# Performance work log

Hardware: AMD Instinct MI355X
Metric: run time of the kernel (lower is better)

## Reference

```python
import jax, jax.numpy as jnp
import numpy as np

B = 128          # batch of proteins
MAX_ATOMS = 16384  # padded max atoms per protein


def setup_inputs() -> dict:
    key = jax.random.key(0)
    k1, k2, k3 = jax.random.split(key, 3)
    # Coordinates are stored flat as [B, 3*MAX_ATOMS] like the torch module.
    inp = jax.random.normal(k1, (B, 3 * MAX_ATOMS), dtype=jnp.float32) * 10.0
    tgt = jax.random.normal(k2, (B, 3 * MAX_ATOMS), dtype=jnp.float32) * 10.0
    num_atoms = jax.random.randint(k3, (B,), MAX_ATOMS // 2, MAX_ATOMS + 1, dtype=jnp.int32)
    return {"input": inp, "target": tgt, "num_atoms": num_atoms}


def _kabsch_rmsd(x_flat, y_flat, num_atoms):
    """Per-batch optimal-superposition RMSD (Kabsch) with ragged atom counts.

    x_flat, y_flat: [B, 3*N] flat coords; num_atoms: [B] valid atoms per row.
    Uses the closed form rmsd^2 = (E0 - 2*(s0 + s1 + d*s2)) / n, where s are
    singular values of the 3x3 cross-covariance and d fixes reflections.
    """
    Bsz, N3 = x_flat.shape
    N = N3 // 3
    x = x_flat.reshape(Bsz, N, 3)
    y = y_flat.reshape(Bsz, N, 3)

    mask = (jnp.arange(N)[None, :] < num_atoms[:, None]).astype(x.dtype)[..., None]  # [B,N,1]
    cnt = num_atoms.astype(x.dtype)[:, None]  # [B,1]

    # Masked centroids and centered (masked) coords.
    xm = jnp.sum(x * mask, axis=1) / cnt  # [B,3]
    ym = jnp.sum(y * mask, axis=1) / cnt
    xc = (x - xm[:, None, :]) * mask      # [B,N,3], zero on padding
    yc = (y - ym[:, None, :]) * mask

    # 3x3 cross-covariance per protein.
    C = jnp.einsum('bni,bnj->bij', xc, yc)  # [B,3,3]

    U, S, Vt = jnp.linalg.svd(C)
    d = jnp.sign(jnp.linalg.det(U) * jnp.linalg.det(Vt))  # reflection correction
    sum_s = S[:, 0] + S[:, 1] + d * S[:, 2]

    E0 = jnp.sum(xc * xc, axis=(1, 2)) + jnp.sum(yc * yc, axis=(1, 2))
    msd = jnp.maximum(E0 - 2.0 * sum_s, 0.0) / cnt[:, 0]
    return jnp.sqrt(msd + 1e-8)  # tiny eps for gradient stability at msd==0


def reference(input, target, num_atoms):
    return _kabsch_rmsd(input, target, num_atoms)
```

## Files before the change

### kernel.cpp

```cpp
#include <hip/hip_runtime.h>

#define NPROT 128
#define NATOMS 16384
#define BLK_PER_PROT 4
#define THREADS 256
#define GROUPS_PER_BLOCK (NATOMS / BLK_PER_PROT / 4)
#define GROUPS_PER_THREAD (GROUPS_PER_BLOCK / THREADS)

__global__ __launch_bounds__(THREADS) void kabsch_reduce_kernel(
    const float* __restrict__ x, const float* __restrict__ y,
    const int* __restrict__ num_atoms, float* __restrict__ ws)
{
    const int b = blockIdx.x / BLK_PER_PROT;
    const int chunk = blockIdx.x % BLK_PER_PROT;
    const int na = num_atoms[b];
    const float4* px = (const float4*)(x + (size_t)b * 3 * NATOMS);
    const float4* py = (const float4*)(y + (size_t)b * 3 * NATOMS);

    float acc[17];
    #pragma unroll
    for (int i = 0; i < 17; ++i) acc[i] = 0.f;

    const int t = threadIdx.x;
    #pragma unroll
    for (int it = 0; it < GROUPS_PER_THREAD; ++it) {
        const int g = chunk * GROUPS_PER_BLOCK + it * THREADS + t;
        const float4 fx0 = px[3 * g + 0];
        const float4 fx1 = px[3 * g + 1];
        const float4 fx2 = px[3 * g + 2];
        const float4 fy0 = py[3 * g + 0];
        const float4 fy1 = py[3 * g + 1];
        const float4 fy2 = py[3 * g + 2];
        const int a0 = g * 4;
        const float xs[4][3] = {{fx0.x, fx0.y, fx0.z}, {fx0.w, fx1.x, fx1.y},
                                {fx1.z, fx1.w, fx2.x}, {fx2.y, fx2.z, fx2.w}};
        const float ys[4][3] = {{fy0.x, fy0.y, fy0.z}, {fy0.w, fy1.x, fy1.y},
                                {fy1.z, fy1.w, fy2.x}, {fy2.y, fy2.z, fy2.w}};
        #pragma unroll
        for (int k = 0; k < 4; ++k) {
            const float m = (a0 + k < na) ? 1.f : 0.f;
            const float X0 = xs[k][0] * m, X1 = xs[k][1] * m, X2 = xs[k][2] * m;
            const float Y0 = ys[k][0] * m, Y1 = ys[k][1] * m, Y2 = ys[k][2] * m;
            acc[0] += X0;  acc[1] += X1;  acc[2] += X2;
            acc[3] += Y0;  acc[4] += Y1;  acc[5] += Y2;
            acc[6]  += X0 * Y0;  acc[7]  += X0 * Y1;  acc[8]  += X0 * Y2;
            acc[9]  += X1 * Y0;  acc[10] += X1 * Y1;  acc[11] += X1 * Y2;
            acc[12] += X2 * Y0;  acc[13] += X2 * Y1;  acc[14] += X2 * Y2;
            acc[15] += X0 * X0 + X1 * X1 + X2 * X2;
            acc[16] += Y0 * Y0 + Y1 * Y1 + Y2 * Y2;
        }
    }

    #pragma unroll
    for (int i = 0; i < 17; ++i) {
        float v = acc[i];
        #pragma unroll
        for (int off = 32; off; off >>= 1) v += __shfl_down(v, off);
        acc[i] = v;
    }
    __shared__ float red[THREADS / 64][17];
    const int wave = t >> 6, lane = t & 63;
    if (lane == 0) {
        #pragma unroll
        for (int i = 0; i < 17; ++i) red[wave][i] = acc[i];
    }
    __syncthreads();
    if (t == 0) {
        float* dst = ws + ((size_t)b * BLK_PER_PROT + chunk) * 17;
        #pragma unroll
        for (int i = 0; i < 17; ++i)
            dst[i] = red[0][i] + red[1][i] + red[2][i] + red[3][i];
    }
}

__global__ __launch_bounds__(NPROT) void kabsch_finalize_kernel(
    const float* __restrict__ ws, const int* __restrict__ num_atoms,
    float* __restrict__ out)
{
    const int b = threadIdx.x;
    if (b >= NPROT) return;

    double s[17];
    #pragma unroll
    for (int i = 0; i < 17; ++i) s[i] = 0.0;
    for (int c = 0; c < BLK_PER_PROT; ++c) {
        const float* p = ws + ((size_t)b * BLK_PER_PROT + c) * 17;
        #pragma unroll
        for (int i = 0; i < 17; ++i) s[i] += (double)p[i];
    }

    const double n = (double)num_atoms[b];
    const double mx0 = s[0] / n, mx1 = s[1] / n, mx2 = s[2] / n;
    const double my0 = s[3] / n, my1 = s[4] / n, my2 = s[5] / n;

    double C00 = s[6]  - n * mx0 * my0, C01 = s[7]  - n * mx0 * my1, C02 = s[8]  - n * mx0 * my2;
    double C10 = s[9]  - n * mx1 * my0, C11 = s[10] - n * mx1 * my1, C12 = s[11] - n * mx1 * my2;
    double C20 = s[12] - n * mx2 * my0, C21 = s[13] - n * mx2 * my1, C22 = s[14] - n * mx2 * my2;

    const double E0 = (s[15] - n * (mx0 * mx0 + mx1 * mx1 + mx2 * mx2))
                    + (s[16] - n * (my0 * my0 + my1 * my1 + my2 * my2));

    const double a00 = C00 * C00 + C10 * C10 + C20 * C20;
    const double a01 = C00 * C01 + C10 * C11 + C20 * C21;
    const double a02 = C00 * C02 + C10 * C12 + C20 * C22;
    const double a11 = C01 * C01 + C11 * C11 + C21 * C21;
    const double a12 = C01 * C02 + C11 * C12 + C21 * C22;
    const double a22 = C02 * C02 + C12 * C12 + C22 * C22;

    const double p1 = a01 * a01 + a02 * a02 + a12 * a12;
    const double q = (a00 + a11 + a22) / 3.0;
    const double b00 = a00 - q, b11 = a11 - q, b22 = a22 - q;
    const double p2 = b00 * b00 + b11 * b11 + b22 * b22 + 2.0 * p1;
    double e0, e1, e2;
    if (p2 <= 0.0) {
        e0 = e1 = e2 = q;
    } else {
        const double p = sqrt(p2 / 6.0);
        const double inv = 1.0 / p;
        const double c00 = b00 * inv, c01 = a01 * inv, c02 = a02 * inv;
        const double c11 = b11 * inv, c12 = a12 * inv, c22 = b22 * inv;
        double r = 0.5 * (c00 * (c11 * c22 - c12 * c12)
                        - c01 * (c01 * c22 - c12 * c02)
                        + c02 * (c01 * c12 - c11 * c02));
        r = fmin(1.0, fmax(-1.0, r));
        const double phi = acos(r) / 3.0;
        e0 = q + 2.0 * p * cos(phi);
        e2 = q + 2.0 * p * cos(phi + 2.0943951023931953);
        e1 = 3.0 * q - e0 - e2;
    }
    const double s0 = sqrt(fmax(e0, 0.0));
    const double s1 = sqrt(fmax(e1, 0.0));
    const double s2 = sqrt(fmax(e2, 0.0));

    const double detC = C00 * (C11 * C22 - C12 * C21)
                      - C01 * (C10 * C22 - C12 * C20)
                      + C02 * (C10 * C21 - C11 * C20);
    const double sum_s = s0 + s1 + (detC < 0.0 ? -s2 : s2);

    const double msd = fmax(E0 - 2.0 * sum_s, 0.0) / n;
    out[b] = (float)sqrt(msd + 1e-8);
}

extern "C" void kernel_launch(void* const* d_in, const int* in_sizes, int n_in,
                              void* d_out, int out_size, void* d_ws, size_t ws_size,
                              hipStream_t stream) {
    const float* x = (const float*)d_in[0];
    const float* y = (const float*)d_in[1];
    const int* num_atoms = (const int*)d_in[2];
    float* out = (float*)d_out;
    float* ws = (float*)d_ws;

    kabsch_reduce_kernel<<<NPROT * BLK_PER_PROT, THREADS, 0, stream>>>(x, y, num_atoms, ws);
    kabsch_finalize_kernel<<<1, NPROT, 0, stream>>>(ws, num_atoms, out);
}
```

Before: 18.70 us.

## Fuse reduction and finalize into one block-per-protein kernel, skip padded atoms

Replaces the two-kernel scheme (4 blocks per protein writing partials, then a single-block finalize) with one 1024-thread block per protein that reduces in shared memory and computes the RMSD in thread 0. This removes the second launch and the workspace round trip. It also skips loading atom groups beyond num_atoms, cutting memory traffic for padding. In exchange only 128 blocks run, which may underuse the GPU's compute units for a bandwidth-bound reduction.

```diff
diff --git a/kernel.cpp b/kernel.cpp
--- a/kernel.cpp
+++ b/kernel.cpp
@@ -2,17 +2,15 @@
 
 #define NPROT 128
 #define NATOMS 16384
-#define BLK_PER_PROT 4
-#define THREADS 256
-#define GROUPS_PER_BLOCK (NATOMS / BLK_PER_PROT / 4)
-#define GROUPS_PER_THREAD (GROUPS_PER_BLOCK / THREADS)
+#define THREADS 1024
+#define WAVES (THREADS / 64)
+#define GROUPS_PER_THREAD (NATOMS / 4 / THREADS)
 
-__global__ __launch_bounds__(THREADS) void kabsch_reduce_kernel(
+__global__ __launch_bounds__(THREADS) void kabsch_onepass_kernel(
     const float* __restrict__ x, const float* __restrict__ y,
-    const int* __restrict__ num_atoms, float* __restrict__ ws)
+    const int* __restrict__ num_atoms, float* __restrict__ out)
 {
-    const int b = blockIdx.x / BLK_PER_PROT;
-    const int chunk = blockIdx.x % BLK_PER_PROT;
+    const int b = blockIdx.x;
     const int na = num_atoms[b];
     const float4* px = (const float4*)(x + (size_t)b * 3 * NATOMS);
     const float4* py = (const float4*)(y + (size_t)b * 3 * NATOMS);
@@ -24,14 +22,15 @@
     const int t = threadIdx.x;
     #pragma unroll
     for (int it = 0; it < GROUPS_PER_THREAD; ++it) {
-        const int g = chunk * GROUPS_PER_BLOCK + it * THREADS + t;
+        const int g = it * THREADS + t;
+        const int a0 = g * 4;
+        if (a0 >= na) continue;
         const float4 fx0 = px[3 * g + 0];
         const float4 fx1 = px[3 * g + 1];
         const float4 fx2 = px[3 * g + 2];
         const float4 fy0 = py[3 * g + 0];
         const float4 fy1 = py[3 * g + 1];
         const float4 fy2 = py[3 * g + 2];
-        const int a0 = g * 4;
         const float xs[4][3] = {{fx0.x, fx0.y, fx0.z}, {fx0.w, fx1.x, fx1.y},
                                 {fx1.z, fx1.w, fx2.x}, {fx2.y, fx2.z, fx2.w}};
         const float ys[4][3] = {{fy0.x, fy0.y, fy0.z}, {fy0.w, fy1.x, fy1.y},
@@ -58,38 +57,30 @@
         for (int off = 32; off; off >>= 1) v += __shfl_down(v, off);
         acc[i] = v;
     }
-    __shared__ float red[THREADS / 64][17];
+    __shared__ float red[WAVES][17];
+    __shared__ double stot[17];
     const int wave = t >> 6, lane = t & 63;
     if (lane == 0) {
         #pragma unroll
         for (int i = 0; i < 17; ++i) red[wave][i] = acc[i];
     }
     __syncthreads();
-    if (t == 0) {
-        float* dst = ws + ((size_t)b * BLK_PER_PROT + chunk) * 17;
+
+    if (t < 17) {
+        double v = 0.0;
         #pragma unroll
-        for (int i = 0; i < 17; ++i)
-            dst[i] = red[0][i] + red[1][i] + red[2][i] + red[3][i];
+        for (int w = 0; w < WAVES; ++w) v += (double)red[w][t];
+        stot[t] = v;
     }
-}
+    __syncthreads();
 
-__global__ __launch_bounds__(NPROT) void kabsch_finalize_kernel(
-    const float* __restrict__ ws, const int* __restrict__ num_atoms,
-    float* __restrict__ out)
-{
-    const int b = threadIdx.x;
-    if (b >= NPROT) return;
+    if (t != 0) return;
 
     double s[17];
     #pragma unroll
-    for (int i = 0; i < 17; ++i) s[i] = 0.0;
-    for (int c = 0; c < BLK_PER_PROT; ++c) {
-        const float* p = ws + ((size_t)b * BLK_PER_PROT + c) * 17;
-        #pragma unroll
-        for (int i = 0; i < 17; ++i) s[i] += (double)p[i];
-    }
+    for (int i = 0; i < 17; ++i) s[i] = stot[i];
 
-    const double n = (double)num_atoms[b];
+    const double n = (double)na;
     const double mx0 = s[0] / n, mx1 = s[1] / n, mx2 = s[2] / n;
     const double my0 = s[3] / n, my1 = s[4] / n, my2 = s[5] / n;
 
@@ -148,8 +139,7 @@
     const float* y = (const float*)d_in[1];
     const int* num_atoms = (const int*)d_in[2];
     float* out = (float*)d_out;
-    float* ws = (float*)d_ws;
+    (void)d_ws; (void)ws_size;
 
-    kabsch_reduce_kernel<<<NPROT * BLK_PER_PROT, THREADS, 0, stream>>>(x, y, num_atoms, ws);
-    kabsch_finalize_kernel<<<1, NPROT, 0, stream>>>(ws, num_atoms, out);
+    kabsch_onepass_kernel<<<NPROT, THREADS, 0, stream>>>(x, y, num_atoms, out);
 }
```

Measured after the change: 16.82 us. 10.0% less time.

## Fuse finalize into reduce via last-block atomic counter and skip padded atoms

Applied to the files above, without the earlier changes.

Merges the two kernels into one: each block writes its partial sums, bumps a per-protein atomic counter, and the last block to arrive computes the 3x3 eigen/RMSD finalize. Atom tiles are interleaved across the four blocks and skipped when beyond num_atoms, so padded memory is never loaded and the load stays balanced. The second kernel launch is replaced by a memset on the counters plus threadfence/atomic overhead, and finalization now runs in scattered single threads instead of one block.

```diff
diff --git a/kernel.cpp b/kernel.cpp
--- a/kernel.cpp
+++ b/kernel.cpp
@@ -4,12 +4,15 @@
 #define NATOMS 16384
 #define BLK_PER_PROT 4
 #define THREADS 256
-#define GROUPS_PER_BLOCK (NATOMS / BLK_PER_PROT / 4)
-#define GROUPS_PER_THREAD (GROUPS_PER_BLOCK / THREADS)
+#define GRID_BLKS (NPROT * BLK_PER_PROT)
+#define TILES 16
+#define TILE_GROUPS 256
+#define COUNTER_OFF_BYTES (36 * 1024)
 
-__global__ __launch_bounds__(THREADS) void kabsch_reduce_kernel(
+__global__ __launch_bounds__(THREADS) void kabsch_fused_kernel(
     const float* __restrict__ x, const float* __restrict__ y,
-    const int* __restrict__ num_atoms, float* __restrict__ ws)
+    const int* __restrict__ num_atoms, float* __restrict__ ws,
+    unsigned int* __restrict__ counters, float* __restrict__ out)
 {
     const int b = blockIdx.x / BLK_PER_PROT;
     const int chunk = blockIdx.x % BLK_PER_PROT;
@@ -23,15 +26,17 @@
 
     const int t = threadIdx.x;
     #pragma unroll
-    for (int it = 0; it < GROUPS_PER_THREAD; ++it) {
-        const int g = chunk * GROUPS_PER_BLOCK + it * THREADS + t;
+    for (int it = 0; it < TILES / BLK_PER_PROT; ++it) {
+        const int tile = it * BLK_PER_PROT + chunk;
+        const int g = tile * TILE_GROUPS + t;
+        const int a0 = g * 4;
+        if (a0 >= na) continue;
         const float4 fx0 = px[3 * g + 0];
         const float4 fx1 = px[3 * g + 1];
         const float4 fx2 = px[3 * g + 2];
         const float4 fy0 = py[3 * g + 0];
         const float4 fy1 = py[3 * g + 1];
         const float4 fy2 = py[3 * g + 2];
-        const int a0 = g * 4;
         const float xs[4][3] = {{fx0.x, fx0.y, fx0.z}, {fx0.w, fx1.x, fx1.y},
                                 {fx1.z, fx1.w, fx2.x}, {fx2.y, fx2.z, fx2.w}};
         const float ys[4][3] = {{fy0.x, fy0.y, fy0.z}, {fy0.w, fy1.x, fy1.y},
@@ -65,31 +70,30 @@
         for (int i = 0; i < 17; ++i) red[wave][i] = acc[i];
     }
     __syncthreads();
-    if (t == 0) {
-        float* dst = ws + ((size_t)b * BLK_PER_PROT + chunk) * 17;
-        #pragma unroll
-        for (int i = 0; i < 17; ++i)
-            dst[i] = red[0][i] + red[1][i] + red[2][i] + red[3][i];
-    }
-}
 
-__global__ __launch_bounds__(NPROT) void kabsch_finalize_kernel(
-    const float* __restrict__ ws, const int* __restrict__ num_atoms,
-    float* __restrict__ out)
-{
-    const int b = threadIdx.x;
-    if (b >= NPROT) return;
+    if (t != 0) return;
+
+    float* dst = ws + ((size_t)b * BLK_PER_PROT + chunk) * 17;
+    #pragma unroll
+    for (int i = 0; i < 17; ++i)
+        dst[i] = red[0][i] + red[1][i] + red[2][i] + red[3][i];
+
+    __threadfence();
+    const unsigned int old = atomicAdd(&counters[b], 1u);
+    if (old != BLK_PER_PROT - 1) return;
+    __threadfence();
 
     double s[17];
     #pragma unroll
     for (int i = 0; i < 17; ++i) s[i] = 0.0;
+    #pragma unroll
     for (int c = 0; c < BLK_PER_PROT; ++c) {
         const float* p = ws + ((size_t)b * BLK_PER_PROT + c) * 17;
         #pragma unroll
         for (int i = 0; i < 17; ++i) s[i] += (double)p[i];
     }
 
-    const double n = (double)num_atoms[b];
+    const double n = (double)na;
     const double mx0 = s[0] / n, mx1 = s[1] / n, mx2 = s[2] / n;
     const double my0 = s[3] / n, my1 = s[4] / n, my2 = s[5] / n;
 
@@ -149,7 +153,8 @@
     const int* num_atoms = (const int*)d_in[2];
     float* out = (float*)d_out;
     float* ws = (float*)d_ws;
+    unsigned int* counters = (unsigned int*)((char*)d_ws + COUNTER_OFF_BYTES);
 
-    kabsch_reduce_kernel<<<NPROT * BLK_PER_PROT, THREADS, 0, stream>>>(x, y, num_atoms, ws);
-    kabsch_finalize_kernel<<<1, NPROT, 0, stream>>>(ws, num_atoms, out);
+    hipMemsetAsync(counters, 0, NPROT * sizeof(unsigned int), stream);
+    kabsch_fused_kernel<<<GRID_BLKS, THREADS, 0, stream>>>(x, y, num_atoms, ws, counters, out);
 }
```

Result: slower. 36.65 us (+96.0%).
